# Kernel optimization log

Measured on AMD Instinct MI355X. Metric: run time of the kernel, lower is better.

## Reference

```python
import jax, jax.numpy as jnp
import numpy as np

B, N, BASE, H, W = 2, 262144, 10, 256, 256
EPS = 1e-9


def setup_inputs() -> dict:
    key = jax.random.key(0)
    kx, ky, kt, kp, kf = jax.random.split(key, 5)
    x = jax.random.uniform(kx, (B, N), minval=0.0, maxval=W - 1.0)
    y = jax.random.uniform(ky, (B, N), minval=0.0, maxval=H - 1.0)
    t = jax.random.uniform(kt, (B, N), minval=0.0, maxval=float(BASE))
    p = jax.random.randint(kp, (B, N), 0, 2).astype(jnp.float32)
    # events: (x, y, t_warp, t_stamp, polarity)
    events = jnp.stack([x, y, t, t, p], axis=-1)
    # flow per temporal bin, channels-last: [B, base, H, W, 2], in pixels/bin
    flow_maps = jax.random.normal(kf, (B, BASE, H, W, 2), dtype=jnp.float32) * 5.0
    return {"events": events, "flow_maps": flow_maps, "base": BASE}


def _bilinear_sample_flow(flow_maps, b_idx, zi, x, y):
    # flow_maps: [b, d, h, w, 2]; border-clamped bilinear sample at float (x, y)
    h, w = flow_maps.shape[2], flow_maps.shape[3]
    x0 = jnp.clip(jnp.floor(x).astype(jnp.int32), 0, w - 2)
    y0 = jnp.clip(jnp.floor(y).astype(jnp.int32), 0, h - 2)
    fx = jnp.clip(x - x0, 0.0, 1.0)
    fy = jnp.clip(y - y0, 0.0, 1.0)
    f00 = flow_maps[b_idx, zi, y0, x0]
    f01 = flow_maps[b_idx, zi, y0, x0 + 1]
    f10 = flow_maps[b_idx, zi, y0 + 1, x0]
    f11 = flow_maps[b_idx, zi, y0 + 1, x0 + 1]
    w00 = ((1 - fx) * (1 - fy))[..., None]
    w01 = (fx * (1 - fy))[..., None]
    w10 = ((1 - fx) * fy)[..., None]
    w11 = (fx * fy)[..., None]
    return w00 * f00 + w01 * f01 + w10 * f10 + w11 * f11  # [b, n, 2]


def _forward(events, flow_maps, base):
    b, n, _ = events.shape
    d, h, w = flow_maps.shape[1], flow_maps.shape[2], flow_maps.shape[3]
    R = base + 1  # number of warp references (all bin edges)
    x, y, t, ts, p = (events[..., i] for i in range(5))
    b_idx = jnp.broadcast_to(jnp.arange(b)[:, None], (b, n))
    zi = jnp.clip(jnp.floor(t).astype(jnp.int32), 0, d - 1)  # event's bin

    # linear 3d warp: sample flow at event location, warp to all R references
    flow = _bilinear_sample_flow(flow_maps, b_idx, zi, x, y)  # [b, n, 2]
    trefs = jnp.arange(R, dtype=events.dtype)
    dt = trefs[None, None, :] - t[..., None]                  # [b, n, R]
    wx = x[..., None] + dt * flow[..., 0:1]
    wy = y[..., None] + dt * flow[..., 1:2]

    # build_iwe: bilinear scatter-add into [b, 2(pol), R, h, w]
    p_idx = jnp.clip(p.astype(jnp.int32), 0, 1)
    chan = (b_idx * 2 + p_idx)[..., None] * R + jnp.arange(R)[None, None, :]
    flat_base = chan * (h * w)                                # [b, n, R]
    x0 = jnp.floor(wx).astype(jnp.int32)
    y0 = jnp.floor(wy).astype(jnp.int32)
    fx = wx - x0
    fy = wy - y0
    tv = jnp.broadcast_to(ts[..., None], wx.shape).ravel()
    iwe = jnp.zeros(b * 2 * R * h * w, dtype=events.dtype)
    iwt = jnp.zeros(b * 2 * R * h * w, dtype=events.dtype)
    corners = ((x0, y0, (1 - fx) * (1 - fy)),
               (x0 + 1, y0, fx * (1 - fy)),
               (x0, y0 + 1, (1 - fx) * fy),
               (x0 + 1, y0 + 1, fx * fy))
    for xi, yi, wc in corners:
        valid = (xi >= 0) & (xi < w) & (yi >= 0) & (yi < h)
        idx = jnp.where(valid, flat_base + yi * w + xi, 0).ravel()
        wv = jnp.where(valid, wc, 0.0).ravel()
        iwe = iwe.at[idx].add(wv)
        iwt = iwt.at[idx].add(wv * tv)
    iwe = iwe.reshape(b, 2, R, h, w)
    iwt = iwt.reshape(b, 2, R, h, w)

    # contrast-maximization loss on image of warped average timestamps
    iwat = iwt / (iwe + EPS)
    inside = (iwe.sum(1) > 0).astype(events.dtype).reshape(b, R, -1).sum(-1) + EPS
    loss = (iwat ** 2).sum(axis=(1, 3, 4))  # neg^2 + pos^2, summed over h*w
    return loss / inside  # [b, R]


def reference(events, flow_maps, base):
    return _forward(events, flow_maps, base)
```

## Files before the change

### kernel.cpp

```cpp
#include <hip/hip_runtime.h>

#define NB 2
#define NN 262144
#define ND 10
#define NR 11
#define HH 256
#define WW 256
#define HWSZ 65536
#define SROWS 8
#define NSTRIP 32
#define PLANE (SROWS * WW)
#define BINS_B (NR * NSTRIP)
#define NBIN (NB * BINS_B)
#define BINCAP (2u * NB * NN * NR)
#define EPSF 1e-9f

#define SC_E 2097152.0f
#define SC_T 524288.0f
#define ISC_E (1.0f / 2097152.0f)
#define ISC_T (1.0f / 524288.0f)


__device__ __forceinline__ unsigned classify(float ax, float ay, float dx, float dy, float rf)
{
    float wx = fmaf(rf, dx, ax);
    float wy = fmaf(rf, dy, ay);
    int xi = (int)floorf(wx);
    int yi = (int)floorf(wy);
    if (xi + 1 < 0 || xi >= WW || yi + 1 < 0 || yi >= HH) return 0xFFu;
    int rr = yi < 0 ? 0 : yi;
    unsigned s = (unsigned)(rr >> 3);
    unsigned str = (yi >= 0 && yi + 1 < HH && ((yi & 7) == 7)) ? 0x40u : 0u;
    return s | str;
}

__global__ __launch_bounds__(1024) void cm_prep(
    const float* __restrict__ events,
    const float* __restrict__ flow,
    float4* __restrict__ rec,
    float* __restrict__ tspol,
    unsigned* __restrict__ counts)
{
    __shared__ unsigned hist[BINS_B];
    for (int i = threadIdx.x; i < BINS_B; i += 1024) hist[i] = 0u;
    __syncthreads();

    int gid = blockIdx.x * 1024 + threadIdx.x;
    int b = gid >> 18;

    const float* e = events + (size_t)gid * 5;
    float x  = e[0];
    float y  = e[1];
    float t  = e[2];
    float ts = e[3];
    float p  = e[4];

    int zi = (int)floorf(t);
    zi = zi < 0 ? 0 : (zi > ND - 1 ? ND - 1 : zi);
    int x0 = (int)floorf(x);
    x0 = x0 < 0 ? 0 : (x0 > WW - 2 ? WW - 2 : x0);
    int y0 = (int)floorf(y);
    y0 = y0 < 0 ? 0 : (y0 > HH - 2 ? HH - 2 : y0);
    float fx = fminf(fmaxf(x - (float)x0, 0.0f), 1.0f);
    float fy = fminf(fmaxf(y - (float)y0, 0.0f), 1.0f);

    const float2* f2 = (const float2*)flow + ((size_t)b * ND + zi) * HWSZ;
    float2 f00 = f2[y0 * WW + x0];
    float2 f01 = f2[y0 * WW + x0 + 1];
    float2 f10 = f2[(y0 + 1) * WW + x0];
    float2 f11 = f2[(y0 + 1) * WW + x0 + 1];
    float w00 = (1.0f - fx) * (1.0f - fy);
    float w01 = fx * (1.0f - fy);
    float w10 = (1.0f - fx) * fy;
    float w11 = fx * fy;
    float dx = w00 * f00.x + w01 * f01.x + w10 * f10.x + w11 * f11.x;
    float dy = w00 * f00.y + w01 * f01.y + w10 * f10.y + w11 * f11.y;
    float ax = fmaf(-t, dx, x);
    float ay = fmaf(-t, dy, y);

    rec[gid] = make_float4(ax, ay, dx, dy);
    int pi = (p != 0.0f) ? 1 : 0;
    tspol[gid] = __int_as_float(__float_as_int(ts) | (pi << 31));

    #pragma unroll
    for (int r = 0; r < NR; ++r) {
        unsigned c = classify(ax, ay, dx, dy, (float)r);
        if (c != 0xFFu) {
            int bin = r * NSTRIP + (int)(c & 31u);
            atomicAdd(&hist[bin], 1u);
            if (c & 0x40u) atomicAdd(&hist[bin + 1], 1u);
        }
    }
    __syncthreads();
    for (int i = threadIdx.x; i < BINS_B; i += 1024) {
        unsigned c = hist[i];
        if (c) atomicAdd(&counts[b * BINS_B + i], c);
    }
}

__global__ __launch_bounds__(1024) void cm_prefix(
    const unsigned* __restrict__ counts,
    unsigned* __restrict__ starts,
    unsigned* __restrict__ cursors)
{
    __shared__ unsigned sa[1024];
    int tid = threadIdx.x;

    unsigned v = (tid < NBIN) ? counts[tid] : 0u;
    sa[tid] = v;
    __syncthreads();
    for (int off = 1; off < 1024; off <<= 1) {
        unsigned x = sa[tid];
        if (tid >= off) x += sa[tid - off];
        __syncthreads();
        sa[tid] = x;
        __syncthreads();
    }
    if (tid < NBIN) {
        unsigned ex = tid ? sa[tid - 1] : 0u;
        starts[tid] = ex;
        cursors[tid] = ex;
    }
    if (tid == 0) starts[NBIN] = sa[NBIN - 1];
}

__global__ __launch_bounds__(1024) void cm_fill(
    const float4* __restrict__ rec,
    const float* __restrict__ tspol,
    unsigned long long* __restrict__ bins,
    unsigned* __restrict__ cursors)
{
    __shared__ unsigned char stash[2048 * NR];
    __shared__ unsigned cnt[BINS_B];
    __shared__ unsigned base[BINS_B];

    for (int i = threadIdx.x; i < BINS_B; i += 1024) cnt[i] = 0u;
    __syncthreads();

    int e0 = blockIdx.x * 2048;
    int b = e0 >> 18;

    float4 ea[2];
    float tp[2];
    #pragma unroll
    for (int k = 0; k < 2; ++k) {
        int el = e0 + k * 1024 + threadIdx.x;
        ea[k] = rec[el];
        tp[k] = tspol[el];
    }

    #pragma unroll
    for (int k = 0; k < 2; ++k) {
        int sl = (k * 1024 + threadIdx.x) * NR;
        for (int r = 0; r < NR; ++r) {
            unsigned c = classify(ea[k].x, ea[k].y, ea[k].z, ea[k].w, (float)r);
            stash[sl + r] = (unsigned char)c;
            if (c != 0xFFu) {
                int bin = r * NSTRIP + (int)(c & 31u);
                atomicAdd(&cnt[bin], 1u);
                if (c & 0x40u) atomicAdd(&cnt[bin + 1], 1u);
            }
        }
    }
    __syncthreads();
    for (int i = threadIdx.x; i < BINS_B; i += 1024) {
        unsigned c = cnt[i];
        base[i] = c ? atomicAdd(&cursors[b * BINS_B + i], c) : 0u;
    }
    __syncthreads();
    for (int i = threadIdx.x; i < BINS_B; i += 1024) cnt[i] = 0u;
    __syncthreads();

    #pragma unroll
    for (int k = 0; k < 2; ++k) {
        int sl = (k * 1024 + threadIdx.x) * NR;
        float tpv = tp[k];
        unsigned pol = (unsigned)__float_as_int(tpv) >> 31;
        float tsv = fabsf(tpv);
        unsigned et = __float2uint_rn(tsv * 65536.0f);
        unsigned long long hdr = ((unsigned long long)et << 43) |
                                 ((unsigned long long)pol << 63);
        for (int r = 0; r < NR; ++r) {
            unsigned c = stash[sl + r];
            if (c != 0xFFu) {
                float rf = (float)r;
                float wx = fmaf(rf, ea[k].z, ea[k].x);
                float wy = fmaf(rf, ea[k].w, ea[k].y);
                int sid = (int)(c & 31u);
                float ty0f = (float)(sid * SROWS);
                unsigned ex = __float2uint_rn((wx + 1.0f) * 32768.0f);
                unsigned ey = __float2uint_rn((wy - ty0f + 1.0f) * 32768.0f);
                unsigned long long ent = hdr | (unsigned long long)ex |
                                         ((unsigned long long)ey << 24);
                int bin = r * NSTRIP + sid;
                unsigned rank = atomicAdd(&cnt[bin], 1u);
                bins[base[bin] + rank] = ent;
                if (c & 0x40u) {
                    unsigned ey2 = __float2uint_rn((wy - ty0f - (float)SROWS + 1.0f) * 32768.0f);
                    unsigned long long ent2 = hdr | (unsigned long long)ex |
                                              ((unsigned long long)ey2 << 24);
                    unsigned rank2 = atomicAdd(&cnt[bin + 1], 1u);
                    bins[base[bin + 1] + rank2] = ent2;
                }
            }
        }
    }
}

__global__ __launch_bounds__(1024) void cm_scan(
    const unsigned long long* __restrict__ bins,
    const unsigned* __restrict__ starts,
    float* __restrict__ accum)
{
    __shared__ unsigned long long acc8[2 * PLANE];
    __shared__ float red[32];

    int blk = blockIdx.x;
    int b  = blk / BINS_B;
    int rm = blk - b * BINS_B;
    int r  = rm >> 5;

    for (int i = threadIdx.x; i < 2 * PLANE; i += 1024) acc8[i] = 0ull;
    __syncthreads();

    unsigned lo = starts[blk];
    unsigned hi = starts[blk + 1];

    auto process = [&](unsigned long long e) {
        float wx  = (float)(unsigned)(e & 0xFFFFFFu) * (1.0f / 32768.0f) - 1.0f;
        float wyr = (float)(unsigned)((e >> 24) & 0x7FFFFu) * (1.0f / 32768.0f) - 1.0f;
        float tsv = (float)(unsigned)((e >> 43) & 0xFFFFFu) * (1.0f / 65536.0f);
        int pi = (int)(e >> 63);
        float fwx = floorf(wx);
        float fwy = floorf(wyr);
        int xi = (int)fwx;
        int yi = (int)fwy;
        float axf = wx - fwx;
        float ayf = wyr - fwy;
        unsigned long long* ap = acc8 + pi * PLANE;
        float c00 = (1.0f - axf) * (1.0f - ayf);
        float c01 = axf * (1.0f - ayf);
        float c10 = (1.0f - axf) * ayf;
        float c11 = axf * ayf;
        #define CM_CORNER(XI, YI, WV)                                          \
            if ((XI) >= 0 && (XI) < WW && (YI) >= 0 && (YI) < SROWS) {         \
                int liq = (YI) * WW + (XI);                                    \
                unsigned pe = __float2uint_rn((WV) * SC_E);                    \
                unsigned pt = __float2uint_rn((WV) * tsv * SC_T);              \
                atomicAdd(&ap[liq],                                            \
                          ((unsigned long long)pt << 32) | (unsigned long long)pe); \
            }
        CM_CORNER(xi,     yi,     c00)
        CM_CORNER(xi + 1, yi,     c01)
        CM_CORNER(xi,     yi + 1, c10)
        CM_CORNER(xi + 1, yi + 1, c11)
        #undef CM_CORNER
    };

    unsigned lo2 = lo + (lo & 1u);
    if ((lo & 1u) && threadIdx.x == 0 && lo < hi) process(bins[lo]);

    const uint4* bv = (const uint4*)bins;
    for (unsigned bse = lo2 + 4u * threadIdx.x; bse < hi; bse += 4096u) {
        uint4 A = bv[bse >> 1];
        uint4 B = bv[(bse >> 1) + 1];
        __builtin_amdgcn_sched_barrier(0);
        unsigned long long e0 = (unsigned long long)A.x | ((unsigned long long)A.y << 32);
        unsigned long long e1 = (unsigned long long)A.z | ((unsigned long long)A.w << 32);
        unsigned long long e2 = (unsigned long long)B.x | ((unsigned long long)B.y << 32);
        unsigned long long e3 = (unsigned long long)B.z | ((unsigned long long)B.w << 32);
        process(e0);
        if (bse + 1 < hi) process(e1);
        if (bse + 2 < hi) process(e2);
        if (bse + 3 < hi) process(e3);
    }
    __syncthreads();

    float ss = 0.0f, ins = 0.0f;
    for (int i = threadIdx.x; i < PLANE; i += 1024) {
        unsigned long long v0 = acc8[i];
        unsigned long long v1 = acc8[PLANE + i];
        unsigned e0i = (unsigned)(v0 & 0xFFFFFFFFull);
        unsigned e1i = (unsigned)(v1 & 0xFFFFFFFFull);
        float e0 = (float)e0i * ISC_E;
        float t0 = (float)(unsigned)(v0 >> 32) * ISC_T;
        float e1 = (float)e1i * ISC_E;
        float t1 = (float)(unsigned)(v1 >> 32) * ISC_T;
        float a0 = t0 / (e0 + EPSF);
        float a1 = t1 / (e1 + EPSF);
        ss += a0 * a0 + a1 * a1;
        ins += ((e0i | e1i) != 0u) ? 1.0f : 0.0f;
    }
    #pragma unroll
    for (int off = 32; off > 0; off >>= 1) {
        ss  += __shfl_down(ss, off, 64);
        ins += __shfl_down(ins, off, 64);
    }
    int lane = threadIdx.x & 63;
    int wv = threadIdx.x >> 6;
    if (lane == 0) { red[2 * wv] = ss; red[2 * wv + 1] = ins; }
    __syncthreads();
    if (threadIdx.x == 0) {
        float tss = 0.0f, tin = 0.0f;
        #pragma unroll
        for (int w = 0; w < 16; ++w) { tss += red[2 * w]; tin += red[2 * w + 1]; }
        int br = b * NR + r;
        atomicAdd(&accum[br * 2],     tss);
        atomicAdd(&accum[br * 2 + 1], tin);
    }
}

__global__ void cm_final(const float* __restrict__ accum, float* __restrict__ out)
{
    int i = threadIdx.x;
    if (i < NB * NR) {
        out[i] = accum[i * 2] / (accum[i * 2 + 1] + EPSF);
    }
}

extern "C" void kernel_launch(void* const* d_in, const int* in_sizes, int n_in,
                              void* d_out, int out_size, void* d_ws, size_t ws_size,
                              hipStream_t stream) {
    const float* events = (const float*)d_in[0];
    const float* flow   = (const float*)d_in[1];

    char* ws = (char*)d_ws;
    size_t off = 0;
    unsigned long long* bins = (unsigned long long*)(ws + off);
    off += (size_t)BINCAP * 8;
    float4* rec = (float4*)(ws + off);         off += (size_t)NB * NN * sizeof(float4);
    float* tspol = (float*)(ws + off);         off += (size_t)NB * NN * sizeof(float);
    unsigned* counts = (unsigned*)(ws + off);  off += NBIN * 4;
    float* accum = (float*)(ws + off);         off += 256;
    unsigned* starts = (unsigned*)(ws + off);  off += (NBIN + 1) * 4 + 60; off &= ~63ull;
    unsigned* cursors = (unsigned*)(ws + off); off += NBIN * 4;

    hipMemsetAsync(counts, 0, NBIN * 4 + 256, stream);

    cm_prep<<<NB * NN / 1024, 1024, 0, stream>>>(events, flow, rec, tspol, counts);

    cm_prefix<<<1, 1024, 0, stream>>>(counts, starts, cursors);

    cm_fill<<<NB * NN / 2048, 1024, 0, stream>>>(rec, tspol, bins, cursors);

    cm_scan<<<NBIN, 1024, 0, stream>>>(bins, starts, accum);

    cm_final<<<1, 64, 0, stream>>>(accum, (float*)d_out);
}
```

Before: 139.9 us.

## Use per-block histograms and offsets to drop fill-pass reclassification and global cursors

cm_prep now writes each block's bin histogram to global memory, and cm_prefix computes per-block exclusive offsets for every bin column plus the global starts. cm_fill uses those offsets directly, so it no longer runs the counting pass, the stash, the global cursor atomics or the extra barriers. cm_final and the memset are folded into cm_scan through a last-block counter, and cm_prefix now zeroes accum and the counter. The cost is a serial 256-step column scan per thread in the single-block prefix kernel, plus extra histogram traffic.

```diff
diff --git a/kernel.cpp b/kernel.cpp
--- a/kernel.cpp
+++ b/kernel.cpp
@@ -13,6 +13,8 @@
 #define BINS_B (NR * NSTRIP)
 #define NBIN (NB * BINS_B)
 #define BINCAP (2u * NB * NN * NR)
+#define NBLK 512
+#define BPB 256
 #define EPSF 1e-9f
 
 #define SC_E 2097152.0f
@@ -39,7 +41,7 @@
     const float* __restrict__ flow,
     float4* __restrict__ rec,
     float* __restrict__ tspol,
-    unsigned* __restrict__ counts)
+    unsigned* __restrict__ hist_g)
 {
     __shared__ unsigned hist[BINS_B];
     for (int i = threadIdx.x; i < BINS_B; i += 1024) hist[i] = 0u;
@@ -92,21 +94,34 @@
         }
     }
     __syncthreads();
-    for (int i = threadIdx.x; i < BINS_B; i += 1024) {
-        unsigned c = hist[i];
-        if (c) atomicAdd(&counts[b * BINS_B + i], c);
-    }
+    for (int i = threadIdx.x; i < BINS_B; i += 1024)
+        hist_g[(size_t)blockIdx.x * BINS_B + i] = hist[i];
 }
 
 __global__ __launch_bounds__(1024) void cm_prefix(
-    const unsigned* __restrict__ counts,
+    const unsigned* __restrict__ hist_g,
+    unsigned* __restrict__ lb,
     unsigned* __restrict__ starts,
-    unsigned* __restrict__ cursors)
+    float* __restrict__ accum,
+    unsigned* __restrict__ ctr)
 {
     __shared__ unsigned sa[1024];
     int tid = threadIdx.x;
 
-    unsigned v = (tid < NBIN) ? counts[tid] : 0u;
+    unsigned v = 0;
+    if (tid < NBIN) {
+        int batch = tid / BINS_B;
+        int bl = tid - batch * BINS_B;
+        const unsigned* hcol = hist_g + (size_t)batch * BPB * BINS_B + bl;
+        unsigned* lcol = lb + (size_t)batch * BPB * BINS_B + bl;
+        unsigned running = 0;
+        #pragma unroll 4
+        for (int g = 0; g < BPB; ++g) {
+            lcol[(size_t)g * BINS_B] = running;
+            running += hcol[(size_t)g * BINS_B];
+        }
+        v = running;
+    }
     sa[tid] = v;
     __syncthreads();
     for (int off = 1; off < 1024; off <<= 1) {
@@ -117,91 +132,62 @@
         __syncthreads();
     }
     if (tid < NBIN) {
-        unsigned ex = tid ? sa[tid - 1] : 0u;
-        starts[tid] = ex;
-        cursors[tid] = ex;
+        starts[tid] = tid ? sa[tid - 1] : 0u;
     }
     if (tid == 0) starts[NBIN] = sa[NBIN - 1];
+    if (tid < 64) accum[tid] = 0.0f;
+    if (tid == 64) *ctr = 0u;
 }
 
 __global__ __launch_bounds__(1024) void cm_fill(
     const float4* __restrict__ rec,
     const float* __restrict__ tspol,
-    unsigned long long* __restrict__ bins,
-    unsigned* __restrict__ cursors)
-{
-    __shared__ unsigned char stash[2048 * NR];
+    const unsigned* __restrict__ lb,
+    const unsigned* __restrict__ starts,
+    unsigned long long* __restrict__ bins)
+{
+    __shared__ unsigned base_l[BINS_B];
     __shared__ unsigned cnt[BINS_B];
-    __shared__ unsigned base[BINS_B];
-
-    for (int i = threadIdx.x; i < BINS_B; i += 1024) cnt[i] = 0u;
-    __syncthreads();
-
-    int e0 = blockIdx.x * 2048;
-    int b = e0 >> 18;
-
-    float4 ea[2];
-    float tp[2];
+
+    int gid = blockIdx.x * 1024 + threadIdx.x;
+    int b = gid >> 18;
+
+    for (int i = threadIdx.x; i < BINS_B; i += 1024) {
+        base_l[i] = starts[b * BINS_B + i] + lb[(size_t)blockIdx.x * BINS_B + i];
+        cnt[i] = 0u;
+    }
+    __syncthreads();
+
+    float4 ea = rec[gid];
+    float tpv = tspol[gid];
+    unsigned pol = (unsigned)__float_as_int(tpv) >> 31;
+    float tsv = fabsf(tpv);
+    unsigned et = __float2uint_rn(tsv * 65536.0f);
+    unsigned long long hdr = ((unsigned long long)et << 43) |
+                             ((unsigned long long)pol << 63);
+
     #pragma unroll
-    for (int k = 0; k < 2; ++k) {
-        int el = e0 + k * 1024 + threadIdx.x;
-        ea[k] = rec[el];
-        tp[k] = tspol[el];
-    }
-
-    #pragma unroll
-    for (int k = 0; k < 2; ++k) {
-        int sl = (k * 1024 + threadIdx.x) * NR;
-        for (int r = 0; r < NR; ++r) {
-            unsigned c = classify(ea[k].x, ea[k].y, ea[k].z, ea[k].w, (float)r);
-            stash[sl + r] = (unsigned char)c;
-            if (c != 0xFFu) {
-                int bin = r * NSTRIP + (int)(c & 31u);
-                atomicAdd(&cnt[bin], 1u);
-                if (c & 0x40u) atomicAdd(&cnt[bin + 1], 1u);
-            }
-        }
-    }
-    __syncthreads();
-    for (int i = threadIdx.x; i < BINS_B; i += 1024) {
-        unsigned c = cnt[i];
-        base[i] = c ? atomicAdd(&cursors[b * BINS_B + i], c) : 0u;
-    }
-    __syncthreads();
-    for (int i = threadIdx.x; i < BINS_B; i += 1024) cnt[i] = 0u;
-    __syncthreads();
-
-    #pragma unroll
-    for (int k = 0; k < 2; ++k) {
-        int sl = (k * 1024 + threadIdx.x) * NR;
-        float tpv = tp[k];
-        unsigned pol = (unsigned)__float_as_int(tpv) >> 31;
-        float tsv = fabsf(tpv);
-        unsigned et = __float2uint_rn(tsv * 65536.0f);
-        unsigned long long hdr = ((unsigned long long)et << 43) |
-                                 ((unsigned long long)pol << 63);
-        for (int r = 0; r < NR; ++r) {
-            unsigned c = stash[sl + r];
-            if (c != 0xFFu) {
-                float rf = (float)r;
-                float wx = fmaf(rf, ea[k].z, ea[k].x);
-                float wy = fmaf(rf, ea[k].w, ea[k].y);
-                int sid = (int)(c & 31u);
-                float ty0f = (float)(sid * SROWS);
-                unsigned ex = __float2uint_rn((wx + 1.0f) * 32768.0f);
-                unsigned ey = __float2uint_rn((wy - ty0f + 1.0f) * 32768.0f);
-                unsigned long long ent = hdr | (unsigned long long)ex |
-                                         ((unsigned long long)ey << 24);
-                int bin = r * NSTRIP + sid;
-                unsigned rank = atomicAdd(&cnt[bin], 1u);
-                bins[base[bin] + rank] = ent;
-                if (c & 0x40u) {
-                    unsigned ey2 = __float2uint_rn((wy - ty0f - (float)SROWS + 1.0f) * 32768.0f);
-                    unsigned long long ent2 = hdr | (unsigned long long)ex |
-                                              ((unsigned long long)ey2 << 24);
-                    unsigned rank2 = atomicAdd(&cnt[bin + 1], 1u);
-                    bins[base[bin + 1] + rank2] = ent2;
-                }
+    for (int r = 0; r < NR; ++r) {
+        unsigned c = classify(ea.x, ea.y, ea.z, ea.w, (float)r);
+        if (c != 0xFFu) {
+            float rf = (float)r;
+            float wx = fmaf(rf, ea.z, ea.x);
+            float wy = fmaf(rf, ea.w, ea.y);
+            int sid = (int)(c & 31u);
+            float ty0f = (float)(sid * SROWS);
+            unsigned ex = __float2uint_rn((wx + 1.0f) * 32768.0f);
+            unsigned ey = __float2uint_rn((wy - ty0f + 1.0f) * 32768.0f);
+            unsigned long long ent = hdr | (unsigned long long)ex |
+                                     ((unsigned long long)ey << 24);
+            int bin = r * NSTRIP + sid;
+            unsigned rank = atomicAdd(&cnt[bin], 1u);
+            bins[base_l[bin] + rank] = ent;
+            if (c & 0x40u) {
+                unsigned ey2 = __float2uint_rn((wy - ty0f - (float)SROWS + 1.0f) * 32768.0f);
+                unsigned long long ent2 = hdr | (unsigned long long)ex |
+                                          ((unsigned long long)ey2 << 24);
+                unsigned rank2 = atomicAdd(&cnt[bin + 1], 1u);
+                bins[base_l[bin + 1] + rank2] = ent2;
             }
         }
     }
@@ -210,7 +196,9 @@
 __global__ __launch_bounds__(1024) void cm_scan(
     const unsigned long long* __restrict__ bins,
     const unsigned* __restrict__ starts,
-    float* __restrict__ accum)
+    float* __restrict__ accum,
+    unsigned* __restrict__ ctr,
+    float* __restrict__ out)
 {
     __shared__ unsigned long long acc8[2 * PLANE];
     __shared__ float red[32];
@@ -307,14 +295,15 @@
         int br = b * NR + r;
         atomicAdd(&accum[br * 2],     tss);
         atomicAdd(&accum[br * 2 + 1], tin);
-    }
-}
-
-__global__ void cm_final(const float* __restrict__ accum, float* __restrict__ out)
-{
-    int i = threadIdx.x;
-    if (i < NB * NR) {
-        out[i] = accum[i * 2] / (accum[i * 2 + 1] + EPSF);
+        __threadfence();
+        unsigned old = atomicAdd(ctr, 1u);
+        red[0] = (old == NBIN - 1) ? 1.0f : 0.0f;
+    }
+    __syncthreads();
+    if (red[0] != 0.0f && threadIdx.x < NB * NR) {
+        float num = atomicAdd(&accum[threadIdx.x * 2],     0.0f);
+        float den = atomicAdd(&accum[threadIdx.x * 2 + 1], 0.0f);
+        out[threadIdx.x] = num / (den + EPSF);
     }
 }
 
@@ -330,20 +319,17 @@
     off += (size_t)BINCAP * 8;
     float4* rec = (float4*)(ws + off);         off += (size_t)NB * NN * sizeof(float4);
     float* tspol = (float*)(ws + off);         off += (size_t)NB * NN * sizeof(float);
-    unsigned* counts = (unsigned*)(ws + off);  off += NBIN * 4;
-    float* accum = (float*)(ws + off);         off += 256;
+    unsigned* hist_g = (unsigned*)(ws + off);  off += (size_t)NBLK * BINS_B * 4;
+    unsigned* lb = (unsigned*)(ws + off);      off += (size_t)NBLK * BINS_B * 4;
     unsigned* starts = (unsigned*)(ws + off);  off += (NBIN + 1) * 4 + 60; off &= ~63ull;
-    unsigned* cursors = (unsigned*)(ws + off); off += NBIN * 4;
-
-    hipMemsetAsync(counts, 0, NBIN * 4 + 256, stream);
-
-    cm_prep<<<NB * NN / 1024, 1024, 0, stream>>>(events, flow, rec, tspol, counts);
-
-    cm_prefix<<<1, 1024, 0, stream>>>(counts, starts, cursors);
-
-    cm_fill<<<NB * NN / 2048, 1024, 0, stream>>>(rec, tspol, bins, cursors);
-
-    cm_scan<<<NBIN, 1024, 0, stream>>>(bins, starts, accum);
-
-    cm_final<<<1, 64, 0, stream>>>(accum, (float*)d_out);
-}
+    float* accum = (float*)(ws + off);         off += 64 * 4;
+    unsigned* ctr = (unsigned*)(ws + off);     off += 64;
+
+    cm_prep<<<NBLK, 1024, 0, stream>>>(events, flow, rec, tspol, hist_g);
+
+    cm_prefix<<<1, 1024, 0, stream>>>(hist_g, lb, starts, accum, ctr);
+
+    cm_fill<<<NBLK, 1024, 0, stream>>>(rec, tspol, lb, starts, bins);
+
+    cm_scan<<<NBIN, 1024, 0, stream>>>(bins, starts, accum, ctr, (float*)d_out);
+}
```

Measured after the change: 157.3 us. 1.12x slower.
